# Performance work log

Measured on AMD Instinct MI355X. Metric: run time of the kernel, lower is better.

## Reference

```python
import jax, jax.numpy as jnp
import numpy as np

# Multi-scale deformable attention core (Deformable DETR MSDeformAttn)
SHAPES = [(180, 180), (90, 90), (45, 45), (23, 23)]  # BEV pyramid; 180*180=32400 matches src slice
LEN = sum(h * w for h, w in SHAPES)  # 43054
D_MODEL, N_HEADS, N_LEVELS, N_POINTS = 256, 8, 4, 4
D_HEAD = D_MODEL // N_HEADS


def setup_inputs() -> dict:
    key = jax.random.key(0)
    ks = jax.random.split(key, 11)
    B = 1
    s = 0.02
    return {
        "query": jax.random.normal(ks[0], (B, LEN, D_MODEL), jnp.float32),
        "value_in": jax.random.normal(ks[1], (B, LEN, D_MODEL), jnp.float32),
        "reference_points": jax.random.uniform(ks[2], (B, LEN, N_LEVELS, 2), jnp.float32),
        "Wv": s * jax.random.normal(ks[3], (D_MODEL, D_MODEL), jnp.float32),
        "bv": jnp.zeros((D_MODEL,), jnp.float32),
        "Ws": s * jax.random.normal(ks[4], (D_MODEL, N_HEADS * N_LEVELS * N_POINTS * 2), jnp.float32),
        "bs": jnp.zeros((N_HEADS * N_LEVELS * N_POINTS * 2,), jnp.float32),
        "Wa": s * jax.random.normal(ks[5], (D_MODEL, N_HEADS * N_LEVELS * N_POINTS), jnp.float32),
        "ba": jnp.zeros((N_HEADS * N_LEVELS * N_POINTS,), jnp.float32),
        "Wo": s * jax.random.normal(ks[6], (D_MODEL, D_MODEL), jnp.float32),
        "bo": jnp.zeros((D_MODEL,), jnp.float32),
    }


def _sample_level(v, loc, Hl, Wl):
    """Bilinear sample (align_corners=False, zero padding) like F.grid_sample.
    v: [B, Hh, Hl*Wl, dh]; loc: [B, Lq, Hh, P, 2] normalized to [0,1].
    Returns [B, Hh, Lq, P, dh]."""
    B, Hh, N, dh = v.shape
    Lq, P = loc.shape[1], loc.shape[3]
    x = loc[..., 0] * Wl - 0.5
    y = loc[..., 1] * Hl - 0.5
    x0 = jnp.floor(x)
    y0 = jnp.floor(y)
    dx = x - x0
    dy = y - y0
    x0i = x0.astype(jnp.int32)
    y0i = y0.astype(jnp.int32)

    def tr(w):  # [B,Lq,Hh,P] -> [B,Hh,Lq,P]
        return jnp.transpose(w, (0, 2, 1, 3))

    def gather(ix, iy):
        valid = ((ix >= 0) & (ix < Wl) & (iy >= 0) & (iy < Hl)).astype(v.dtype)
        idx = jnp.clip(iy, 0, Hl - 1) * Wl + jnp.clip(ix, 0, Wl - 1)  # [B,Lq,Hh,P]
        idx_t = jnp.transpose(idx, (0, 2, 1, 3)).reshape(B, Hh, Lq * P)
        g = jnp.take_along_axis(v, idx_t[..., None], axis=2).reshape(B, Hh, Lq, P, dh)
        return g * tr(valid)[..., None]

    out = (gather(x0i, y0i) * tr((1 - dx) * (1 - dy))[..., None]
           + gather(x0i + 1, y0i) * tr(dx * (1 - dy))[..., None]
           + gather(x0i, y0i + 1) * tr((1 - dx) * dy)[..., None]
           + gather(x0i + 1, y0i + 1) * tr(dx * dy)[..., None])
    return out


def reference(query, value_in, reference_points, Wv, bv, Ws, bs, Wa, ba, Wo, bo):
    B, Lq, _ = query.shape
    # value projection -> [B, Len, Hh, dh]
    value = (value_in @ Wv + bv).reshape(B, LEN, N_HEADS, D_HEAD)
    # sampling offsets [B,Lq,Hh,L,P,2]
    offsets = (query @ Ws + bs).reshape(B, Lq, N_HEADS, N_LEVELS, N_POINTS, 2)
    # attention weights, softmax over L*P
    attn = jax.nn.softmax((query @ Wa + ba).reshape(B, Lq, N_HEADS, N_LEVELS * N_POINTS), axis=-1)
    attn = attn.reshape(B, Lq, N_HEADS, N_LEVELS, N_POINTS)
    # normalized sampling locations
    normalizer = jnp.array([[w, h] for h, w in SHAPES], jnp.float32)  # [L,2] as (W,H)
    loc = (reference_points[:, :, None, :, None, :]
           + offsets / normalizer[None, None, None, :, None, :])  # [B,Lq,Hh,L,P,2]

    acc = jnp.zeros((B, N_HEADS, Lq, D_HEAD), query.dtype)
    start = 0
    for lvl, (Hl, Wl) in enumerate(SHAPES):
        v = jnp.transpose(value[:, start:start + Hl * Wl], (0, 2, 1, 3))  # [B,Hh,N,dh]
        samp = _sample_level(v, loc[:, :, :, lvl], Hl, Wl)  # [B,Hh,Lq,P,dh]
        w = jnp.transpose(attn[:, :, :, lvl], (0, 2, 1, 3))  # [B,Hh,Lq,P]
        acc = acc + jnp.sum(samp * w[..., None], axis=3)
        start += Hl * Wl
    out = jnp.transpose(acc, (0, 2, 1, 3)).reshape(B, Lq, D_MODEL)
    return out @ Wo + bo
```

## Files before the change

kernel.cpp:

```cpp
#include <hip/hip_runtime.h>
#include <hip/hip_bf16.h>
#include <cstddef>

#define QLEN 43054

typedef __attribute__((ext_vector_type(8))) short short8;
typedef __attribute__((ext_vector_type(8))) unsigned short ushort8;
typedef __attribute__((ext_vector_type(4))) float f32x4;

__device__ __forceinline__ unsigned short f32_to_bf16_rne(float f) {
    unsigned int u = __float_as_uint(f);
    unsigned int r = (u + 0x7fffu + ((u >> 16) & 1u)) >> 16;
    return (unsigned short)r;
}
__device__ __forceinline__ float bf16_to_f32(unsigned short h) {
    return __uint_as_float(((unsigned int)h) << 16);
}

__global__ __launch_bounds__(256) void w_split(
    const float* __restrict__ W, unsigned short* __restrict__ hi,
    unsigned short* __restrict__ lo, int N)
{
    const int t = blockIdx.x * 256 + threadIdx.x;
    const int n = t >> 8;
    const int k = t & 255;
    const float w = W[(size_t)k * N + n];
    const unsigned short h = f32_to_bf16_rne(w);
    const float rem = w - bf16_to_f32(h);
    hi[(size_t)n * 256 + k] = h;
    lo[(size_t)n * 256 + k] = f32_to_bf16_rne(rem);
}

__global__ __launch_bounds__(256) void cvt_bf16(
    const float* __restrict__ in, unsigned short* __restrict__ out, int n4)
{
    int i = blockIdx.x * 256 + threadIdx.x;
    const int stride = gridDim.x * 256;
    for (; i < n4; i += stride) {
        const float4 v = ((const float4*)in)[i];
        ushort4 o;
        o.x = f32_to_bf16_rne(v.x);
        o.y = f32_to_bf16_rne(v.y);
        o.z = f32_to_bf16_rne(v.z);
        o.w = f32_to_bf16_rne(v.w);
        ((ushort4*)out)[i] = o;
    }
}

__global__ __launch_bounds__(256) void gemm_mfma_lds(
    const unsigned short* __restrict__ A,
    const unsigned short* __restrict__ Bh,
    const unsigned short* __restrict__ Bl,
    const float* __restrict__ bias,
    float* __restrict__ Cf, unsigned short* __restrict__ Cb,
    int M, int N, int mode)
{
    __shared__ alignas(16) unsigned short As[128 * 32];
    __shared__ alignas(16) unsigned short Bhs[128 * 32];
    __shared__ alignas(16) unsigned short Bls[128 * 32];

    const int tid = threadIdx.x;
    const int lane = tid & 63;
    const int w = tid >> 6;
    const int wm = (w >> 1) * 64;
    const int wn = (w & 1) * 64;
    const int bm = blockIdx.x * 128;
    const int bn = blockIdx.y * 128;

    const int rl = lane >> 2;
    const int cd = lane & 3;

    const int fr = lane & 15;
    const int fc = lane >> 4;

    f32x4 acc[4][4];
    #pragma unroll
    for (int i = 0; i < 4; ++i)
        #pragma unroll
        for (int j = 0; j < 4; ++j)
            acc[i][j] = (f32x4){0.f, 0.f, 0.f, 0.f};

    for (int k0 = 0; k0 < 256; k0 += 32) {
        #pragma unroll
        for (int i = 0; i < 2; ++i) {
            const int ii = w * 2 + i;
            const int row = ii * 16 + rl;
            const int cs = cd ^ ((row >> 1) & 3);
            const size_t gof = (size_t)(k0 + cs * 8);
            const int ra = min(bm + row, M - 1);
            const int rb = bn + row;
            __builtin_amdgcn_global_load_lds(
                (const unsigned int*)(A + (size_t)ra * 256 + gof),
                (unsigned int*)&As[ii * 512], 16, 0, 0);
            __builtin_amdgcn_global_load_lds(
                (const unsigned int*)(Bh + (size_t)rb * 256 + gof),
                (unsigned int*)&Bhs[ii * 512], 16, 0, 0);
            __builtin_amdgcn_global_load_lds(
                (const unsigned int*)(Bl + (size_t)rb * 256 + gof),
                (unsigned int*)&Bls[ii * 512], 16, 0, 0);
        }
        __syncthreads();

        short8 a[4], bh4[4], bl4[4];
        #pragma unroll
        for (int f = 0; f < 4; ++f) {
            const int rowA = wm + f * 16 + fr;
            const int pcA = fc ^ ((rowA >> 1) & 3);
            a[f] = *(const short8*)&As[rowA * 32 + pcA * 8];
            const int rowB = wn + f * 16 + fr;
            const int pcB = fc ^ ((rowB >> 1) & 3);
            bh4[f] = *(const short8*)&Bhs[rowB * 32 + pcB * 8];
            bl4[f] = *(const short8*)&Bls[rowB * 32 + pcB * 8];
        }

        #pragma unroll
        for (int i = 0; i < 4; ++i)
            #pragma unroll
            for (int j = 0; j < 4; ++j) {
                acc[i][j] = __builtin_amdgcn_mfma_f32_16x16x32_bf16(a[i], bh4[j], acc[i][j], 0, 0, 0);
                acc[i][j] = __builtin_amdgcn_mfma_f32_16x16x32_bf16(a[i], bl4[j], acc[i][j], 0, 0, 0);
            }
        __syncthreads();
    }

    float bv[4];
    #pragma unroll
    for (int j = 0; j < 4; ++j) bv[j] = bias[bn + wn + j * 16 + fr];

    const int rbase = bm + wm + fc * 4;
    if (mode == 0) {
        #pragma unroll
        for (int i = 0; i < 4; ++i)
            #pragma unroll
            for (int r = 0; r < 4; ++r) {
                const int row = rbase + i * 16 + r;
                if (row < M) {
                    #pragma unroll
                    for (int j = 0; j < 4; ++j) {
                        const int col = bn + wn + j * 16 + fr;
                        Cf[(size_t)row * N + col] = acc[i][j][r] + bv[j];
                    }
                }
            }
    } else {
        #pragma unroll
        for (int i = 0; i < 4; ++i)
            #pragma unroll
            for (int r = 0; r < 4; ++r) {
                const int row = rbase + i * 16 + r;
                if (row < M) {
                    #pragma unroll
                    for (int j = 0; j < 4; ++j) {
                        const int col = bn + wn + j * 16 + fr;
                        Cb[(size_t)row * 256 + col] = f32_to_bf16_rne(acc[i][j][r] + bv[j]);
                    }
                }
            }
    }
}

__global__ __launch_bounds__(256) void msda_sample(
    const unsigned short* __restrict__ value,
    const float* __restrict__ offs,
    const float* __restrict__ attl,
    const float* __restrict__ refp,
    unsigned short* __restrict__ tmp)
{
    const int wv = (blockIdx.x << 2) + (threadIdx.x >> 6);
    const int lane = threadIdx.x & 63;
    const int q = wv >> 3;
    const int h = wv & 7;
    if (q >= QLEN) return;

    const int g = lane >> 2;
    const int j = lane & 3;

    const float offv  = offs[(size_t)q * 256 + h * 32 + (lane & 31)];
    const float logit = attl[(size_t)q * 128 + h * 16 + (lane & 15)];
    const float refv  = refp[(size_t)q * 8 + (lane & 7)];

    float mx = logit;
    #pragma unroll
    for (int msk = 1; msk < 16; msk <<= 1) mx = fmaxf(mx, __shfl_xor(mx, msk));
    const float e = __expf(logit - mx);
    float sm = e;
    #pragma unroll
    for (int msk = 1; msk < 16; msk <<= 1) sm += __shfl_xor(sm, msk);
    const float attw = e / sm;

    const int lvl = g >> 2;
    const int LW = (lvl == 0) ? 180 : (lvl == 1) ? 90 : (lvl == 2) ? 45 : 23;
    const int LS = (lvl == 0) ? 0 : (lvl == 1) ? 32400 : (lvl == 2) ? 40500 : 42525;

    const float ox = __shfl(offv, g * 2);
    const float oy = __shfl(offv, g * 2 + 1);
    const float aw = __shfl(attw, g);
    const float rx = __shfl(refv, lvl * 2);
    const float ry = __shfl(refv, lvl * 2 + 1);

    const float fLW = (float)LW;
    const float x = fmaf(rx, fLW, ox) - 0.5f;
    const float y = fmaf(ry, fLW, oy) - 0.5f;
    const float x0f = floorf(x), y0f = floorf(y);
    const float dx = x - x0f, dy = y - y0f;
    const int x0 = (int)x0f, y0 = (int)y0f;
    const int x1 = x0 + 1, y1 = y0 + 1;

    const bool vx0 = (x0 >= 0) && (x0 < LW);
    const bool vx1 = (x1 >= 0) && (x1 < LW);
    const bool vy0 = (y0 >= 0) && (y0 < LW);
    const bool vy1 = (y1 >= 0) && (y1 < LW);

    const int x0c = min(max(x0, 0), LW - 1);
    const int x1c = min(max(x1, 0), LW - 1);
    const int y0c = min(max(y0, 0), LW - 1);
    const int y1c = min(max(y1, 0), LW - 1);

    const float wx0 = 1.f - dx, wy0 = 1.f - dy;
    float w00 = wx0 * wy0 * aw;
    float w10 = dx  * wy0 * aw;
    float w01 = wx0 * dy  * aw;
    float w11 = dx  * dy  * aw;
    w00 = (vx0 && vy0) ? w00 : 0.f;
    w10 = (vx1 && vy0) ? w10 : 0.f;
    w01 = (vx0 && vy1) ? w01 : 0.f;
    w11 = (vx1 && vy1) ? w11 : 0.f;

    const unsigned short* __restrict__ vb = value + h * 32 + j * 8;
    const int r0 = LS + y0c * LW;
    const int r1 = LS + y1c * LW;
    const ushort8 v00 = *(const ushort8*)(vb + (size_t)(r0 + x0c) * 256);
    const ushort8 v10 = *(const ushort8*)(vb + (size_t)(r0 + x1c) * 256);
    const ushort8 v01 = *(const ushort8*)(vb + (size_t)(r1 + x0c) * 256);
    const ushort8 v11 = *(const ushort8*)(vb + (size_t)(r1 + x1c) * 256);

    float acc[8];
    #pragma unroll
    for (int e2 = 0; e2 < 8; ++e2) {
        float s = w00 * bf16_to_f32(v00[e2]);
        s = fmaf(w10, bf16_to_f32(v10[e2]), s);
        s = fmaf(w01, bf16_to_f32(v01[e2]), s);
        s = fmaf(w11, bf16_to_f32(v11[e2]), s);
        acc[e2] = s;
    }

    #pragma unroll
    for (int msk = 4; msk <= 32; msk <<= 1)
        #pragma unroll
        for (int e2 = 0; e2 < 8; ++e2)
            acc[e2] += __shfl_xor(acc[e2], msk);

    if (g == 0) {
        ushort8 o;
        #pragma unroll
        for (int e2 = 0; e2 < 8; ++e2) o[e2] = f32_to_bf16_rne(acc[e2]);
        *(ushort8*)(tmp + (size_t)q * 256 + h * 32 + j * 8) = o;
    }
}

extern "C" void kernel_launch(void* const* d_in, const int* in_sizes, int n_in,
                              void* d_out, int out_size, void* d_ws, size_t ws_size,
                              hipStream_t stream)
{
    const float* query    = (const float*)d_in[0];
    const float* value_in = (const float*)d_in[1];
    const float* refp     = (const float*)d_in[2];
    const float* Wv = (const float*)d_in[3];
    const float* bv = (const float*)d_in[4];
    const float* Ws = (const float*)d_in[5];
    const float* bs = (const float*)d_in[6];
    const float* Wa = (const float*)d_in[7];
    const float* ba = (const float*)d_in[8];
    const float* Wo = (const float*)d_in[9];
    const float* bo = (const float*)d_in[10];
    float* out = (float*)d_out;

    char* p = (char*)d_ws;
    const size_t SZ_BF = (size_t)QLEN * 256 * 2;
    unsigned short* q_bf   = (unsigned short*)p;               p += SZ_BF;
    unsigned short* vin_bf = (unsigned short*)p;               p += SZ_BF;
    unsigned short* val_bf = (unsigned short*)p;               p += SZ_BF;
    float*          offs   = (float*)p;                        p += (size_t)QLEN * 256 * 4;
    float*          attl   = (float*)p;                        p += (size_t)QLEN * 128 * 4;
    unsigned short* wtv_h  = (unsigned short*)p;               p += 256 * 256 * 2;
    unsigned short* wtv_l  = (unsigned short*)p;               p += 256 * 256 * 2;
    unsigned short* wts_h  = (unsigned short*)p;               p += 256 * 256 * 2;
    unsigned short* wts_l  = (unsigned short*)p;               p += 256 * 256 * 2;
    unsigned short* wta_h  = (unsigned short*)p;               p += 128 * 256 * 2;
    unsigned short* wta_l  = (unsigned short*)p;               p += 128 * 256 * 2;
    unsigned short* wto_h  = (unsigned short*)p;               p += 256 * 256 * 2;
    unsigned short* wto_l  = (unsigned short*)p;               p += 256 * 256 * 2;
    unsigned short* tmp_bf = vin_bf;

    const dim3 blk(256);
    const int MT = (QLEN + 127) / 128;
    const int n4 = QLEN * 256 / 4;

    w_split<<<256, blk, 0, stream>>>(Wv, wtv_h, wtv_l, 256);
    w_split<<<256, blk, 0, stream>>>(Ws, wts_h, wts_l, 256);
    w_split<<<128, blk, 0, stream>>>(Wa, wta_h, wta_l, 128);
    w_split<<<256, blk, 0, stream>>>(Wo, wto_h, wto_l, 256);
    cvt_bf16<<<1024, blk, 0, stream>>>(query,    q_bf,   n4);
    cvt_bf16<<<1024, blk, 0, stream>>>(value_in, vin_bf, n4);

    gemm_mfma_lds<<<dim3(MT, 2), blk, 0, stream>>>(vin_bf, wtv_h, wtv_l, bv,
                                                   nullptr, val_bf, QLEN, 256, 1);
    gemm_mfma_lds<<<dim3(MT, 2), blk, 0, stream>>>(q_bf, wts_h, wts_l, bs,
                                                   offs, nullptr, QLEN, 256, 0);
    gemm_mfma_lds<<<dim3(MT, 1), blk, 0, stream>>>(q_bf, wta_h, wta_l, ba,
                                                   attl, nullptr, QLEN, 128, 0);

    const int nwaves = QLEN * 8;
    msda_sample<<<dim3((nwaves + 3) / 4), blk, 0, stream>>>(val_bf, offs, attl, refp, tmp_bf);

    gemm_mfma_lds<<<dim3(MT, 2), blk, 0, stream>>>(tmp_bf, wto_h, wto_l, bo,
                                                   out, nullptr, QLEN, 256, 0);
}
```

Measured before the change: 411.7 us.

## Fuse weight-split and convert kernels, merge offset/attn GEMMs, double-buffer GEMM LDS

```diff
diff --git a/kernel.cpp b/kernel.cpp
--- a/kernel.cpp
+++ b/kernel.cpp
@@ -7,6 +7,13 @@
 typedef __attribute__((ext_vector_type(8))) short short8;
 typedef __attribute__((ext_vector_type(8))) unsigned short ushort8;
 typedef __attribute__((ext_vector_type(4))) float f32x4;
+
+#if defined(__has_builtin)
+#if __has_builtin(__builtin_amdgcn_fdot2_f32_bf16)
+#define MSDA_DOT2 1
+typedef __attribute__((ext_vector_type(2))) __bf16 bf16x2;
+#endif
+#endif
 
 __device__ __forceinline__ unsigned short f32_to_bf16_rne(float f) {
     unsigned int u = __float_as_uint(f);
@@ -17,47 +24,74 @@
     return __uint_as_float(((unsigned int)h) << 16);
 }
 
-__global__ __launch_bounds__(256) void w_split(
-    const float* __restrict__ W, unsigned short* __restrict__ hi,
-    unsigned short* __restrict__ lo, int N)
-{
-    const int t = blockIdx.x * 256 + threadIdx.x;
-    const int n = t >> 8;
-    const int k = t & 255;
-    const float w = W[(size_t)k * N + n];
-    const unsigned short h = f32_to_bf16_rne(w);
-    const float rem = w - bf16_to_f32(h);
-    hi[(size_t)n * 256 + k] = h;
-    lo[(size_t)n * 256 + k] = f32_to_bf16_rne(rem);
-}
-
-__global__ __launch_bounds__(256) void cvt_bf16(
-    const float* __restrict__ in, unsigned short* __restrict__ out, int n4)
-{
+__global__ __launch_bounds__(256) void w_split_all(
+    const float* __restrict__ Wv, const float* __restrict__ Ws,
+    const float* __restrict__ Wa, const float* __restrict__ Wo,
+    unsigned short* __restrict__ wtv_h, unsigned short* __restrict__ wtv_l,
+    unsigned short* __restrict__ wtsa_h, unsigned short* __restrict__ wtsa_l,
+    unsigned short* __restrict__ wto_h, unsigned short* __restrict__ wto_l)
+{
+    const int b = blockIdx.x;
+    const int tid = threadIdx.x;
+    const float* W; unsigned short *hi, *lo; int N, n0add = 0, t;
+    if (b < 64)       { W = Wv; hi = wtv_h;  lo = wtv_l;  N = 256; t = b; }
+    else if (b < 128) { W = Ws; hi = wtsa_h; lo = wtsa_l; N = 256; t = b - 64; }
+    else if (b < 160) { W = Wa; hi = wtsa_h; lo = wtsa_l; N = 128; t = b - 128; n0add = 256; }
+    else              { W = Wo; hi = wto_h;  lo = wto_l;  N = 256; t = b - 160; }
+    const int kt = t & 7, nt = t >> 3;
+    const int k0 = kt * 32, n0 = nt * 32;
+
+    __shared__ float T[32][33];
+    const int r = tid >> 3;
+    const int c4 = (tid & 7) * 4;
+    const float4 v = *(const float4*)(W + (size_t)(k0 + r) * N + n0 + c4);
+    T[r][c4 + 0] = v.x; T[r][c4 + 1] = v.y; T[r][c4 + 2] = v.z; T[r][c4 + 3] = v.w;
+    __syncthreads();
+
+    const int n = r;
+    ushort4 oh, ol;
+    #pragma unroll
+    for (int i = 0; i < 4; ++i) {
+        const float w = T[c4 + i][n];
+        const unsigned short h = f32_to_bf16_rne(w);
+        ((unsigned short*)&oh)[i] = h;
+        ((unsigned short*)&ol)[i] = f32_to_bf16_rne(w - bf16_to_f32(h));
+    }
+    const size_t ob = (size_t)(n0add + n0 + n) * 256 + k0 + c4;
+    *(ushort4*)(hi + ob) = oh;
+    *(ushort4*)(lo + ob) = ol;
+}
+
+__global__ __launch_bounds__(256) void cvt_all(
+    const float* __restrict__ a, const float* __restrict__ b,
+    unsigned short* __restrict__ oa, unsigned short* __restrict__ ob)
+{
+    const int n4 = QLEN * 64;
     int i = blockIdx.x * 256 + threadIdx.x;
     const int stride = gridDim.x * 256;
-    for (; i < n4; i += stride) {
-        const float4 v = ((const float4*)in)[i];
+    for (; i < 2 * n4; i += stride) {
+        const float4 v = (i < n4) ? ((const float4*)a)[i] : ((const float4*)b)[i - n4];
         ushort4 o;
         o.x = f32_to_bf16_rne(v.x);
         o.y = f32_to_bf16_rne(v.y);
         o.z = f32_to_bf16_rne(v.z);
         o.w = f32_to_bf16_rne(v.w);
-        ((ushort4*)out)[i] = o;
-    }
-}
-
-__global__ __launch_bounds__(256) void gemm_mfma_lds(
+        if (i < n4) ((ushort4*)oa)[i] = o;
+        else        ((ushort4*)ob)[i - n4] = o;
+    }
+}
+
+__global__ __launch_bounds__(256) void gemm_mfma_db(
     const unsigned short* __restrict__ A,
     const unsigned short* __restrict__ Bh,
     const unsigned short* __restrict__ Bl,
-    const float* __restrict__ bias,
+    const float* __restrict__ bias1, const float* __restrict__ bias2,
     float* __restrict__ Cf, unsigned short* __restrict__ Cb,
-    int M, int N, int mode)
-{
-    __shared__ alignas(16) unsigned short As[128 * 32];
-    __shared__ alignas(16) unsigned short Bhs[128 * 32];
-    __shared__ alignas(16) unsigned short Bls[128 * 32];
+    int M, int N, int n1, int mode)
+{
+    __shared__ alignas(16) unsigned short As[2][4096];
+    __shared__ alignas(16) unsigned short Bhs[2][4096];
+    __shared__ alignas(16) unsigned short Bls[2][4096];
 
     const int tid = threadIdx.x;
     const int lane = tid & 63;
@@ -69,48 +103,54 @@
 
     const int rl = lane >> 2;
     const int cd = lane & 3;
-
     const int fr = lane & 15;
     const int fc = lane >> 4;
 
-    f32x4 acc[4][4];
-    #pragma unroll
-    for (int i = 0; i < 4; ++i)
-        #pragma unroll
-        for (int j = 0; j < 4; ++j)
-            acc[i][j] = (f32x4){0.f, 0.f, 0.f, 0.f};
-
-    for (int k0 = 0; k0 < 256; k0 += 32) {
+    auto stage = [&](int buf, int k0) {
         #pragma unroll
         for (int i = 0; i < 2; ++i) {
             const int ii = w * 2 + i;
             const int row = ii * 16 + rl;
             const int cs = cd ^ ((row >> 1) & 3);
-            const size_t gof = (size_t)(k0 + cs * 8);
+            const size_t gof = (size_t)k0 + cs * 8;
             const int ra = min(bm + row, M - 1);
             const int rb = bn + row;
             __builtin_amdgcn_global_load_lds(
                 (const unsigned int*)(A + (size_t)ra * 256 + gof),
-                (unsigned int*)&As[ii * 512], 16, 0, 0);
+                (unsigned int*)&As[buf][ii * 512], 16, 0, 0);
             __builtin_amdgcn_global_load_lds(
                 (const unsigned int*)(Bh + (size_t)rb * 256 + gof),
-                (unsigned int*)&Bhs[ii * 512], 16, 0, 0);
+                (unsigned int*)&Bhs[buf][ii * 512], 16, 0, 0);
             __builtin_amdgcn_global_load_lds(
                 (const unsigned int*)(Bl + (size_t)rb * 256 + gof),
-                (unsigned int*)&Bls[ii * 512], 16, 0, 0);
+                (unsigned int*)&Bls[buf][ii * 512], 16, 0, 0);
         }
-        __syncthreads();
+    };
+
+    f32x4 acc[4][4];
+    #pragma unroll
+    for (int i = 0; i < 4; ++i)
+        #pragma unroll
+        for (int j = 0; j < 4; ++j)
+            acc[i][j] = (f32x4){0.f, 0.f, 0.f, 0.f};
+
+    stage(0, 0);
+    __syncthreads();
+    int cur = 0;
+
+    for (int t = 0; t < 8; ++t) {
+        if (t < 7) stage(cur ^ 1, (t + 1) * 32);
 
         short8 a[4], bh4[4], bl4[4];
         #pragma unroll
         for (int f = 0; f < 4; ++f) {
             const int rowA = wm + f * 16 + fr;
             const int pcA = fc ^ ((rowA >> 1) & 3);
-            a[f] = *(const short8*)&As[rowA * 32 + pcA * 8];
+            a[f] = *(const short8*)&As[cur][rowA * 32 + pcA * 8];
             const int rowB = wn + f * 16 + fr;
             const int pcB = fc ^ ((rowB >> 1) & 3);
-            bh4[f] = *(const short8*)&Bhs[rowB * 32 + pcB * 8];
-            bl4[f] = *(const short8*)&Bls[rowB * 32 + pcB * 8];
+            bh4[f] = *(const short8*)&Bhs[cur][rowB * 32 + pcB * 8];
+            bl4[f] = *(const short8*)&Bls[cur][rowB * 32 + pcB * 8];
         }
 
         #pragma unroll
@@ -120,12 +160,16 @@
                 acc[i][j] = __builtin_amdgcn_mfma_f32_16x16x32_bf16(a[i], bh4[j], acc[i][j], 0, 0, 0);
                 acc[i][j] = __builtin_amdgcn_mfma_f32_16x16x32_bf16(a[i], bl4[j], acc[i][j], 0, 0, 0);
             }
-        __syncthreads();
+
+        if (t < 7) { __syncthreads(); cur ^= 1; }
     }
 
     float bv[4];
     #pragma unroll
-    for (int j = 0; j < 4; ++j) bv[j] = bias[bn + wn + j * 16 + fr];
+    for (int j = 0; j < 4; ++j) {
+        const int col = bn + wn + j * 16 + fr;
+        bv[j] = (col < n1) ? bias1[col] : bias2[col - n1];
+    }
 
     const int rbase = bm + wm + fc * 4;
     if (mode == 0) {
@@ -161,8 +205,7 @@
 
 __global__ __launch_bounds__(256) void msda_sample(
     const unsigned short* __restrict__ value,
-    const float* __restrict__ offs,
-    const float* __restrict__ attl,
+    const float* __restrict__ oa,
     const float* __restrict__ refp,
     unsigned short* __restrict__ tmp)
 {
@@ -175,8 +218,8 @@
     const int g = lane >> 2;
     const int j = lane & 3;
 
-    const float offv  = offs[(size_t)q * 256 + h * 32 + (lane & 31)];
-    const float logit = attl[(size_t)q * 128 + h * 16 + (lane & 15)];
+    const float offv  = oa[(size_t)q * 384 + h * 32 + (lane & 31)];
+    const float logit = oa[(size_t)q * 384 + 256 + h * 16 + (lane & 15)];
     const float refv  = refp[(size_t)q * 8 + (lane & 7)];
 
     float mx = logit;
@@ -186,7 +229,7 @@
     float sm = e;
     #pragma unroll
     for (int msk = 1; msk < 16; msk <<= 1) sm += __shfl_xor(sm, msk);
-    const float attw = e / sm;
+    const float attw = e * __builtin_amdgcn_rcpf(sm);
 
     const int lvl = g >> 2;
     const int LW = (lvl == 0) ? 180 : (lvl == 1) ? 90 : (lvl == 2) ? 45 : 23;
@@ -229,12 +272,44 @@
     const unsigned short* __restrict__ vb = value + h * 32 + j * 8;
     const int r0 = LS + y0c * LW;
     const int r1 = LS + y1c * LW;
+
+    float acc[8];
+
+#ifdef MSDA_DOT2
+    const uint4 u00 = *(const uint4*)(vb + (size_t)(r0 + x0c) * 256);
+    const uint4 u10 = *(const uint4*)(vb + (size_t)(r0 + x1c) * 256);
+    const uint4 u01 = *(const uint4*)(vb + (size_t)(r1 + x0c) * 256);
+    const uint4 u11 = *(const uint4*)(vb + (size_t)(r1 + x1c) * 256);
+    const unsigned int U00[4] = {u00.x, u00.y, u00.z, u00.w};
+    const unsigned int U10[4] = {u10.x, u10.y, u10.z, u10.w};
+    const unsigned int U01[4] = {u01.x, u01.y, u01.z, u01.w};
+    const unsigned int U11[4] = {u11.x, u11.y, u11.z, u11.w};
+
+    const unsigned int wau =
+        ((unsigned int)f32_to_bf16_rne(w10) << 16) | f32_to_bf16_rne(w00);
+    const unsigned int wbu =
+        ((unsigned int)f32_to_bf16_rne(w11) << 16) | f32_to_bf16_rne(w01);
+    const bf16x2 WA = __builtin_bit_cast(bf16x2, wau);
+    const bf16x2 WB = __builtin_bit_cast(bf16x2, wbu);
+
+    #pragma unroll
+    for (int e2 = 0; e2 < 4; ++e2) {
+        const unsigned p_lo = __builtin_amdgcn_perm(U10[e2], U00[e2], 0x05040100u);
+        const unsigned p_hi = __builtin_amdgcn_perm(U10[e2], U00[e2], 0x07060302u);
+        const unsigned q_lo = __builtin_amdgcn_perm(U11[e2], U01[e2], 0x05040100u);
+        const unsigned q_hi = __builtin_amdgcn_perm(U11[e2], U01[e2], 0x07060302u);
+        float s0 = __builtin_amdgcn_fdot2_f32_bf16(__builtin_bit_cast(bf16x2, p_lo), WA, 0.f, false);
+        s0 = __builtin_amdgcn_fdot2_f32_bf16(__builtin_bit_cast(bf16x2, q_lo), WB, s0, false);
+        float s1 = __builtin_amdgcn_fdot2_f32_bf16(__builtin_bit_cast(bf16x2, p_hi), WA, 0.f, false);
+        s1 = __builtin_amdgcn_fdot2_f32_bf16(__builtin_bit_cast(bf16x2, q_hi), WB, s1, false);
+        acc[2 * e2] = s0;
+        acc[2 * e2 + 1] = s1;
+    }
+#else
     const ushort8 v00 = *(const ushort8*)(vb + (size_t)(r0 + x0c) * 256);
     const ushort8 v10 = *(const ushort8*)(vb + (size_t)(r0 + x1c) * 256);
     const ushort8 v01 = *(const ushort8*)(vb + (size_t)(r1 + x0c) * 256);
     const ushort8 v11 = *(const ushort8*)(vb + (size_t)(r1 + x1c) * 256);
-
-    float acc[8];
     #pragma unroll
     for (int e2 = 0; e2 < 8; ++e2) {
         float s = w00 * bf16_to_f32(v00[e2]);
@@ -243,6 +318,7 @@
         s = fmaf(w11, bf16_to_f32(v11[e2]), s);
         acc[e2] = s;
     }
+#endif
 
     #pragma unroll
     for (int msk = 4; msk <= 32; msk <<= 1)
@@ -277,42 +353,33 @@
 
     char* p = (char*)d_ws;
     const size_t SZ_BF = (size_t)QLEN * 256 * 2;
-    unsigned short* q_bf   = (unsigned short*)p;               p += SZ_BF;
-    unsigned short* vin_bf = (unsigned short*)p;               p += SZ_BF;
-    unsigned short* val_bf = (unsigned short*)p;               p += SZ_BF;
-    float*          offs   = (float*)p;                        p += (size_t)QLEN * 256 * 4;
-    float*          attl   = (float*)p;                        p += (size_t)QLEN * 128 * 4;
-    unsigned short* wtv_h  = (unsigned short*)p;               p += 256 * 256 * 2;
-    unsigned short* wtv_l  = (unsigned short*)p;               p += 256 * 256 * 2;
-    unsigned short* wts_h  = (unsigned short*)p;               p += 256 * 256 * 2;
-    unsigned short* wts_l  = (unsigned short*)p;               p += 256 * 256 * 2;
-    unsigned short* wta_h  = (unsigned short*)p;               p += 128 * 256 * 2;
-    unsigned short* wta_l  = (unsigned short*)p;               p += 128 * 256 * 2;
-    unsigned short* wto_h  = (unsigned short*)p;               p += 256 * 256 * 2;
-    unsigned short* wto_l  = (unsigned short*)p;               p += 256 * 256 * 2;
+    unsigned short* q_bf   = (unsigned short*)p;  p += SZ_BF;
+    unsigned short* vin_bf = (unsigned short*)p;  p += SZ_BF;
+    unsigned short* val_bf = (unsigned short*)p;  p += SZ_BF;
+    float*          oaB    = (float*)p;           p += (size_t)QLEN * 384 * 4;
+    unsigned short* wtv_h  = (unsigned short*)p;  p += 256 * 256 * 2;
+    unsigned short* wtv_l  = (unsigned short*)p;  p += 256 * 256 * 2;
+    unsigned short* wtsa_h = (unsigned short*)p;  p += 384 * 256 * 2;
+    unsigned short* wtsa_l = (unsigned short*)p;  p += 384 * 256 * 2;
+    unsigned short* wto_h  = (unsigned short*)p;  p += 256 * 256 * 2;
+    unsigned short* wto_l  = (unsigned short*)p;  p += 256 * 256 * 2;
     unsigned short* tmp_bf = vin_bf;
 
     const dim3 blk(256);
     const int MT = (QLEN + 127) / 128;
-    const int n4 = QLEN * 256 / 4;
-
-    w_split<<<256, blk, 0, stream>>>(Wv, wtv_h, wtv_l, 256);
-    w_split<<<256, blk, 0, stream>>>(Ws, wts_h, wts_l, 256);
-    w_split<<<128, blk, 0, stream>>>(Wa, wta_h, wta_l, 128);
-    w_split<<<256, blk, 0, stream>>>(Wo, wto_h, wto_l, 256);
-    cvt_bf16<<<1024, blk, 0, stream>>>(query,    q_bf,   n4);
-    cvt_bf16<<<1024, blk, 0, stream>>>(value_in, vin_bf, n4);
-
-    gemm_mfma_lds<<<dim3(MT, 2), blk, 0, stream>>>(vin_bf, wtv_h, wtv_l, bv,
-                                                   nullptr, val_bf, QLEN, 256, 1);
-    gemm_mfma_lds<<<dim3(MT, 2), blk, 0, stream>>>(q_bf, wts_h, wts_l, bs,
-                                                   offs, nullptr, QLEN, 256, 0);
-    gemm_mfma_lds<<<dim3(MT, 1), blk, 0, stream>>>(q_bf, wta_h, wta_l, ba,
-                                                   attl, nullptr, QLEN, 128, 0);
+
+    w_split_all<<<224, blk, 0, stream>>>(Wv, Ws, Wa, Wo, wtv_h, wtv_l,
+                                         wtsa_h, wtsa_l, wto_h, wto_l);
+    cvt_all<<<2048, blk, 0, stream>>>(query, value_in, q_bf, vin_bf);
+
+    gemm_mfma_db<<<dim3(MT, 2), blk, 0, stream>>>(vin_bf, wtv_h, wtv_l, bv, bv,
+                                                  nullptr, val_bf, QLEN, 256, 256, 1);
+    gemm_mfma_db<<<dim3(MT, 3), blk, 0, stream>>>(q_bf, wtsa_h, wtsa_l, bs, ba,
+                                                  oaB, nullptr, QLEN, 384, 256, 0);
 
     const int nwaves = QLEN * 8;
-    msda_sample<<<dim3((nwaves + 3) / 4), blk, 0, stream>>>(val_bf, offs, attl, refp, tmp_bf);
-
-    gemm_mfma_lds<<<dim3(MT, 2), blk, 0, stream>>>(tmp_bf, wto_h, wto_l, bo,
-                                                   out, nullptr, QLEN, 256, 0);
-}
+    msda_sample<<<dim3((nwaves + 3) / 4), blk, 0, stream>>>(val_bf, oaB, refp, tmp_bf);
+
+    gemm_mfma_db<<<dim3(MT, 2), blk, 0, stream>>>(tmp_bf, wto_h, wto_l, bo, bo,
+                                                  out, nullptr, QLEN, 256, 256, 0);
+}
```

New measurement: 376.7 us. 1.09x faster.
